# Optimization experiments

Hardware: AMD Instinct MI355X
Metric: run time of the kernel (lower is better)

## Reference

```python
import jax, jax.numpy as jnp
import numpy as np

N_QUBITS = 12
LAYERS = 3


def _apply(state, mats, axes):
    """Apply batched k-qubit gate. state: [B]+[2]*n complex64; mats: [B, 2^k, 2^k]; axes: state axes (1-based)."""
    k = len(axes)
    d = 2 ** k
    s = jnp.moveaxis(state, axes, tuple(range(1, k + 1)))
    shp = s.shape
    s = jnp.einsum('bij,bjk->bik', mats, s.reshape(shp[0], d, -1))
    return jnp.moveaxis(s.reshape(shp), tuple(range(1, k + 1)), axes)


def _ry(theta):
    # RY(theta) = [[cos(t/2), -sin(t/2)], [sin(t/2), cos(t/2)]], batched over B
    c = jnp.cos(theta / 2).astype(jnp.complex64)
    s = jnp.sin(theta / 2).astype(jnp.complex64)
    return jnp.stack([jnp.stack([c, -s], -1), jnp.stack([s, c], -1)], -2)


def _crx(theta):
    # CRX: identity on control=0 subspace, RX(theta) on control=1 subspace (basis order |ct>)
    c = jnp.cos(theta / 2).astype(jnp.complex64)
    s = (-1j) * jnp.sin(theta / 2).astype(jnp.complex64)
    o = jnp.ones_like(c)
    z = jnp.zeros_like(c)
    rows = [[o, z, z, z], [z, o, z, z], [z, z, c, s], [z, z, s, c]]
    return jnp.stack([jnp.stack(r, -1) for r in rows], -2)


def _circuit(state_re, state_im, params):
    B = params.shape[0]
    n = N_QUBITS
    state = (state_re + 1j * state_im).astype(jnp.complex64).reshape((B,) + (2,) * n)
    p = params.reshape(B, LAYERS, 4, n)  # param idx order: RY block, CRX block, RY block, CRX block
    for l in range(LAYERS):
        th = p[:, l]
        for w in range(n):
            state = _apply(state, _ry(th[:, 0, w]), (w + 1,))
        for i, w in enumerate(reversed(range(n))):
            state = _apply(state, _crx(th[:, 1, i]), (w + 1, ((w + 1) % n) + 1))
        for w in range(n):
            state = _apply(state, _ry(th[:, 2, w]), (w + 1,))
        for i, w in enumerate([n - 1] + list(range(n - 1))):
            state = _apply(state, _crx(th[:, 3, i]), (w + 1, ((w - 1) % n) + 1))
    state = state.reshape(B, -1)
    return jnp.stack([state.real, state.imag], -1)  # [B, 2^n, 2]


def setup_inputs() -> dict:
    key = jax.random.key(0)
    k1, k2, k3 = jax.random.split(key, 3)
    B = 128
    dim = 2 ** N_QUBITS
    return {
        'state_re': jax.random.normal(k1, (B, dim), jnp.float32),
        'state_im': jax.random.normal(k2, (B, dim), jnp.float32),
        'params': jax.random.normal(k3, (B, LAYERS * 4 * N_QUBITS), jnp.float32),
    }


def reference(state_re, state_im, params):
    return _circuit(state_re, state_im, params)
```

## Files before the change

### kernel.cpp

```cpp
#include <hip/hip_runtime.h>
#include <math.h>

#define DIM  4096
#define BLK  256
#define NPAR 144

typedef float v2f __attribute__((ext_vector_type(2)));

struct Ph { int reg[4]; int wav[2]; };
struct TMap { unsigned pk[8]; unsigned short so[16]; unsigned short rn[16]; };

constexpr int REGS[12][4] = {
  {8,9,10,11},
  {4,5,6,7},
  {0,1,2,3},
  {0,1,2,11},
  {2,3,4,5},
  {5,6,7,8},
  {8,9,10,11},
  {4,5,6,7},
  {0,1,10,11},
  {7,8,9,10},
  {4,5,6,7},
  {1,2,3,4}
};

constexpr Ph mkPh(int idx) {
  int l = idx / 12, e = idx % 12;
  Ph p = {};
  for (int j = 0; j < 4; ++j) p.reg[j] = REGS[e][j];
  int w0, w1;
  if (e == 11 || (l > 0 && e == 0)) { w0 = 0; w1 = 5; }
  else if (l == 0 && e <= 1)        { w0 = 0; w1 = 1; }
  else if (e <= 5)                  { w0 = 9; w1 = 10; }
  else                              { w0 = 2; w1 = 3; }
  p.wav[0] = w0; p.wav[1] = w1;
  return p;
}
constexpr Ph phaseAt(int i) {
  if (i == 0 || i == 37) { Ph p = {{0,1,2,3},{10,11}}; return p; }
  return mkPh(i - 1);
}
constexpr bool inArr(const int* a, int n, int b) {
  for (int i = 0; i < n; ++i) if (a[i] == b) return true;
  return false;
}
constexpr bool isLoc(int t) {
  if (t == 0 || t == 36) return false;
  Ph a = phaseAt(t), b = phaseAt(t + 1);
  return a.wav[0] == b.wav[0] && a.wav[1] == b.wav[1];
}
constexpr int bufIdx(int t) {
  int k = 0;
  for (int u = 0; u <= t; ++u) if (!isLoc(u)) ++k;
  return (k + 1) & 1;
}

struct BuildOut { TMap m; bool ok; };

constexpr BuildOut buildT(Ph o, Ph n, bool local) {
  BuildOut R = {};
  R.ok = true;
  bool lo[12] = {}, ln[12] = {};
  for (int b = 0; b < 12; ++b) {
    lo[b] = !inArr(o.reg, 4, b) && !inArr(o.wav, 2, b);
    ln[b] = !inArr(n.reg, 4, b) && !inArr(n.wav, 2, b);
  }
  int col[12] = {};
  bool uo[12] = {}, un[12] = {}, inBank[12] = {}, pairA[12] = {};
  int row = 0;
  for (int b = 0; b < 12 && row < 4; ++b)
    if (lo[b] && ln[b]) { col[b] |= 1 << row; uo[b] = un[b] = true; inBank[b] = true; ++row; }
  while (row < 4) {
    int a = -1, c = -1;
    for (int b = 0; b < 12; ++b) if (lo[b] && !uo[b]) { a = b; break; }
    for (int b = 0; b < 12; ++b) if (ln[b] && !un[b]) { c = b; break; }
    if (a < 0 || c < 0) { R.ok = false; return R; }
    col[a] |= 1 << row; col[c] |= 1 << row;
    uo[a] = true; un[c] = true; inBank[a] = true; inBank[c] = true; pairA[a] = true;
    ++row;
  }
  bool idset[12] = {};
  int nid = 0;
  for (int b = 0; b < 12; ++b) { idset[b] = !inBank[b] || pairA[b]; if (idset[b]) ++nid; }
  if (nid != 8) { R.ok = false; return R; }
  if (local) {
    if (!idset[o.wav[0]] || !idset[o.wav[1]]) { R.ok = false; return R; }
    col[o.wav[0]] |= 1 << 10; col[o.wav[1]] |= 1 << 11;
    idset[o.wav[0]] = idset[o.wav[1]] = false;
    int rr = 4;
    for (int b = 0; b < 12; ++b) if (idset[b]) { col[b] |= 1 << rr; ++rr; }
    if (rr != 10) { R.ok = false; return R; }
  } else {
    int rr = 4;
    for (int b = 0; b < 12; ++b) if (idset[b]) { col[b] |= 1 << rr; ++rr; }
    if (rr != 12) { R.ok = false; return R; }
  }
  {
    int pv[12] = {}, pb[12] = {};
    int nr = 0;
    for (int b = 0; b < 12; ++b) {
      int v = col[b];
      for (int k = 0; k < nr; ++k) if (v & pb[k]) v ^= pv[k];
      if (v) { pb[nr] = v & (-v); pv[nr] = v; ++nr; }
    }
    if (nr != 12) { R.ok = false; return R; }
  }
  int Lo[6] = {}, Ln[6] = {};
  int i0 = 0, i1 = 0;
  for (int b = 0; b < 12; ++b) { if (lo[b]) Lo[i0++] = b; if (ln[b]) Ln[i1++] = b; }
  for (int i = 0; i < 8; ++i) {
    unsigned po = (i < 6) ? (unsigned)col[Lo[i]] : (unsigned)col[o.wav[i - 6]];
    unsigned pn = (i < 6) ? (unsigned)col[Ln[i]] : (unsigned)col[n.wav[i - 6]];
    R.m.pk[i] = po | (pn << 16);
  }
  for (int r = 0; r < 16; ++r) {
    int s = 0, t = 0;
    for (int j = 0; j < 4; ++j)
      if ((r >> j) & 1) { s ^= col[o.reg[j]]; t ^= col[n.reg[j]]; }
    R.m.so[r] = (unsigned short)(s * 8);
    R.m.rn[r] = (unsigned short)(t * 8);
  }
  return R;
}

struct AllT { TMap t[37]; bool loc[37]; int buf[37]; bool ok; };
constexpr AllT buildAll() {
  AllT A = {};
  A.ok = true;
  for (int t = 0; t < 37; ++t) {
    BuildOut b = buildT(phaseAt(t), phaseAt(t + 1), isLoc(t));
    A.t[t] = b.m;
    A.ok = A.ok && b.ok;
    A.loc[t] = isLoc(t);
    A.buf[t] = bufIdx(t);
  }
  return A;
}
constexpr AllT AT = buildAll();
static_assert(AT.ok, "slot-map construction failed");

template<int J>
__device__ __forceinline__ void ry16(v2f (&z)[16], v2f a) {
  const float c = a.x, s = a.y;
  #pragma unroll
  for (int p = 0; p < 8; ++p) {
    const int r0 = ((p & ~((1 << J) - 1)) << 1) | (p & ((1 << J) - 1));
    const int r1 = r0 | (1 << J);
    v2f u = z[r0], v = z[r1];
    z[r0] = c * u - s * v;
    z[r1] = s * u + c * v;
  }
}
template<int JC, int JT>
__device__ __forceinline__ void crx16(v2f (&z)[16], v2f a) {
  const float c = a.x, s = a.y;
  constexpr int MC = 1 << JC, MT = 1 << JT;
  constexpr int mlo = MC < MT ? MC : MT;
  constexpr int mhi = MC < MT ? MT : MC;
  #pragma unroll
  for (int p = 0; p < 4; ++p) {
    int q = ((p & ~(mlo - 1)) << 1) | (p & (mlo - 1));
    q = ((q & ~(mhi - 1)) << 1) | (q & (mhi - 1));
    const int r0 = q | MC, r1 = r0 | MT;
    v2f u = z[r0], v = z[r1];
    v2f n0, n1;
    n0.x = c * u.x + s * v.y;
    n0.y = c * u.y - s * v.x;
    n1.x = c * v.x + s * u.y;
    n1.y = c * v.y - s * u.x;
    z[r0] = n0; z[r1] = n1;
  }
}

template<int E>
__device__ __forceinline__ void gates(v2f (&z)[16], const v2f* ang, int base) {
  auto A = [&](int k) { return ang[base + k]; };
  if constexpr (E == 0)      { ry16<0>(z,A(3));  ry16<1>(z,A(2));  ry16<2>(z,A(1));  ry16<3>(z,A(0)); }
  else if constexpr (E == 1) { ry16<0>(z,A(7));  ry16<1>(z,A(6));  ry16<2>(z,A(5));  ry16<3>(z,A(4)); }
  else if constexpr (E == 2) { ry16<0>(z,A(11)); ry16<1>(z,A(10)); ry16<2>(z,A(9));  ry16<3>(z,A(8)); }
  else if constexpr (E == 3) { crx16<0,3>(z,A(12)); crx16<1,0>(z,A(13)); crx16<2,1>(z,A(14)); }
  else if constexpr (E == 4) { crx16<1,0>(z,A(15)); crx16<2,1>(z,A(16)); crx16<3,2>(z,A(17)); }
  else if constexpr (E == 5) { crx16<1,0>(z,A(18)); crx16<2,1>(z,A(19)); crx16<3,2>(z,A(20)); }
  else if constexpr (E == 6) { crx16<1,0>(z,A(21)); crx16<2,1>(z,A(22)); crx16<3,2>(z,A(23));
                               ry16<0>(z,A(27)); ry16<1>(z,A(26)); }
  else if constexpr (E == 7) { ry16<0>(z,A(31)); ry16<1>(z,A(30)); ry16<2>(z,A(29)); ry16<3>(z,A(28)); }
  else if constexpr (E == 8) { ry16<2>(z,A(25)); ry16<3>(z,A(24)); ry16<0>(z,A(35)); ry16<1>(z,A(34));
                               crx16<0,1>(z,A(36)); crx16<3,0>(z,A(37)); crx16<2,3>(z,A(38)); }
  else if constexpr (E == 9) { crx16<2,3>(z,A(39)); crx16<1,2>(z,A(40)); crx16<0,1>(z,A(41)); }
  else if constexpr (E == 10){ crx16<2,3>(z,A(42)); crx16<1,2>(z,A(43)); crx16<0,1>(z,A(44)); }
  else                       { ry16<1>(z,A(33)); ry16<2>(z,A(32));
                               crx16<2,3>(z,A(45)); crx16<1,2>(z,A(46)); crx16<0,1>(z,A(47)); }
}

template<int T>
__device__ __forceinline__ void restage(v2f (&z)[16], int tid, char* Lb, char* C0, char* C1) {
  constexpr bool LOC = AT.loc[T];
  char* buf = LOC ? Lb : (AT.buf[T] ? C1 : C0);
  unsigned acc = 0;
  #pragma unroll
  for (int i = 0; i < 8; ++i)
    acc ^= (unsigned)(-((tid >> i) & 1)) & AT.t[T].pk[i];
  const unsigned bo = (acc & 0xfffu) << 3;
  const unsigned bn = ((acc >> 16) & 0xfffu) << 3;
  #pragma unroll
  for (int r = 0; r < 16; ++r)
    *(v2f*)(buf + (bo ^ AT.t[T].so[r])) = z[r];
  if (LOC) { asm volatile("s_waitcnt lgkmcnt(0)" ::: "memory"); }
  else     { __syncthreads(); }
  #pragma unroll
  for (int r = 0; r < 16; ++r)
    z[r] = *(const v2f*)(buf + (bn ^ AT.t[T].rn[r]));
}

template<int L>
__device__ __forceinline__ void layer(v2f (&z)[16], int tid, const v2f* ang,
                                      char* Lb, char* C0, char* C1) {
  const int base = 48 * L;
  gates<0>(z, ang, base);  restage<12*L + 1>(z, tid, Lb, C0, C1);
  gates<1>(z, ang, base);  restage<12*L + 2>(z, tid, Lb, C0, C1);
  gates<2>(z, ang, base);  restage<12*L + 3>(z, tid, Lb, C0, C1);
  gates<3>(z, ang, base);  restage<12*L + 4>(z, tid, Lb, C0, C1);
  gates<4>(z, ang, base);  restage<12*L + 5>(z, tid, Lb, C0, C1);
  gates<5>(z, ang, base);  restage<12*L + 6>(z, tid, Lb, C0, C1);
  gates<6>(z, ang, base);  restage<12*L + 7>(z, tid, Lb, C0, C1);
  gates<7>(z, ang, base);  restage<12*L + 8>(z, tid, Lb, C0, C1);
  gates<8>(z, ang, base);  restage<12*L + 9>(z, tid, Lb, C0, C1);
  gates<9>(z, ang, base);  restage<12*L + 10>(z, tid, Lb, C0, C1);
  gates<10>(z, ang, base); restage<12*L + 11>(z, tid, Lb, C0, C1);
  gates<11>(z, ang, base);
  if constexpr (L < 2) restage<12*L + 12>(z, tid, Lb, C0, C1);
}

__global__ __launch_bounds__(BLK) void ansatz_kernel(
    const float* __restrict__ sre, const float* __restrict__ sim,
    const float* __restrict__ params, float* __restrict__ out) {

  __shared__ v2f C0s[DIM], C1s[DIM], Ls[DIM];
  __shared__ v2f ang[NPAR];

  const int b = blockIdx.x, tid = threadIdx.x;
  char* C0 = (char*)C0s;
  char* C1 = (char*)C1s;
  char* Lb = (char*)Ls;

  if (tid < NPAR) {
    float s, c;
    sincosf(0.5f * params[b * NPAR + tid], &s, &c);
    v2f a; a.x = c; a.y = s;
    ang[tid] = a;
  }

  v2f z[16];
  {
    const float4* pr = (const float4*)(sre + b * DIM + (tid << 4));
    const float4* pi = (const float4*)(sim + b * DIM + (tid << 4));
    float4 fr[4], fi[4];
    #pragma unroll
    for (int k = 0; k < 4; ++k) { fr[k] = pr[k]; fi[k] = pi[k]; }
    unsigned acc = 0;
    #pragma unroll
    for (int i = 0; i < 8; ++i)
      acc ^= (unsigned)(-((tid >> i) & 1)) & AT.t[0].pk[i];
    const unsigned bo = (acc & 0xfffu) << 3;
    const unsigned bn = ((acc >> 16) & 0xfffu) << 3;
    #pragma unroll
    for (int r = 0; r < 16; ++r) {
      const float* f0 = (const float*)&fr[r >> 2];
      const float* f1 = (const float*)&fi[r >> 2];
      v2f v; v.x = f0[r & 3]; v.y = f1[r & 3];
      *(v2f*)(C0 + (bo ^ AT.t[0].so[r])) = v;
    }
    __syncthreads();
    #pragma unroll
    for (int r = 0; r < 16; ++r)
      z[r] = *(const v2f*)(C0 + (bn ^ AT.t[0].rn[r]));
  }

  layer<0>(z, tid, ang, Lb, C0, C1);
  layer<1>(z, tid, ang, Lb, C0, C1);
  layer<2>(z, tid, ang, Lb, C0, C1);

  {
    unsigned acc = 0;
    #pragma unroll
    for (int i = 0; i < 8; ++i)
      acc ^= (unsigned)(-((tid >> i) & 1)) & AT.t[36].pk[i];
    const unsigned bo = (acc & 0xfffu) << 3;
    const unsigned bn = ((acc >> 16) & 0xfffu) << 3;
    char* buf = AT.buf[36] ? C1 : C0;
    #pragma unroll
    for (int r = 0; r < 16; ++r)
      *(v2f*)(buf + (bo ^ AT.t[36].so[r])) = z[r];
    __syncthreads();
    v2f* o2 = (v2f*)out + (size_t)b * DIM + (tid << 4);
    #pragma unroll
    for (int r = 0; r < 16; r += 2) {
      v2f v0 = *(const v2f*)(buf + (bn ^ AT.t[36].rn[r]));
      v2f v1 = *(const v2f*)(buf + (bn ^ AT.t[36].rn[r + 1]));
      float4 w; w.x = v0.x; w.y = v0.y; w.z = v1.x; w.w = v1.y;
      *(float4*)(o2 + r) = w;
    }
  }
}

extern "C" void kernel_launch(void* const* d_in, const int* in_sizes, int n_in,
                              void* d_out, int out_size, void* d_ws, size_t ws_size,
                              hipStream_t stream) {
  const float* sre    = (const float*)d_in[0];
  const float* sim    = (const float*)d_in[1];
  const float* params = (const float*)d_in[2];
  float* out          = (float*)d_out;

  const int B = in_sizes[0] / DIM;
  ansatz_kernel<<<B, BLK, 0, stream>>>(sre, sim, params, out);
}
```

Baseline: 90.67 us.

## Split state across 512 threads with 3-qubit register phases

Doubles the block size to 512 threads so each thread holds 8 amplitudes (3 register qubits) instead of 16, with three wave-level qubits instead of two. The phase schedule is redesigned around sliding 3-qubit windows, so each phase applies a few RY/CRX gates before restaging through shared memory, and the compile-time slot-map builder is generalised to match. This exposes more parallelism per block and cuts register pressure. In exchange there are the same number of restage phases, each doing less arithmetic, so LDS traffic and barrier cost per gate rise relative to compute.

```diff
diff --git a/kernel.cpp b/kernel.cpp
--- a/kernel.cpp
+++ b/kernel.cpp
@@ -2,44 +2,30 @@
 #include <math.h>
 
 #define DIM  4096
-#define BLK  256
+#define BLK  512
 #define NPAR 144
 
 typedef float v2f __attribute__((ext_vector_type(2)));
 
-struct Ph { int reg[4]; int wav[2]; };
-struct TMap { unsigned pk[8]; unsigned short so[16]; unsigned short rn[16]; };
-
-constexpr int REGS[12][4] = {
-  {8,9,10,11},
-  {4,5,6,7},
-  {0,1,2,3},
-  {0,1,2,11},
-  {2,3,4,5},
-  {5,6,7,8},
-  {8,9,10,11},
-  {4,5,6,7},
-  {0,1,10,11},
-  {7,8,9,10},
-  {4,5,6,7},
-  {1,2,3,4}
-};
-
-constexpr Ph mkPh(int idx) {
-  int l = idx / 12, e = idx % 12;
+struct Ph { int reg[3]; int wav[3]; };
+struct TMap { unsigned pk[9]; unsigned short so[8]; unsigned short rn[8]; };
+
+constexpr int REGS[12][3] = {
+  {11,0,1},{1,2,3},{3,4,5},{5,6,7},{7,8,9},{9,10,11},
+  {11,0,1},{9,10,11},{7,8,9},{5,6,7},{3,4,5},{1,2,3}};
+
+constexpr Ph phaseAt(int i) {
   Ph p = {};
-  for (int j = 0; j < 4; ++j) p.reg[j] = REGS[e][j];
-  int w0, w1;
-  if (e == 11 || (l > 0 && e == 0)) { w0 = 0; w1 = 5; }
-  else if (l == 0 && e <= 1)        { w0 = 0; w1 = 1; }
-  else if (e <= 5)                  { w0 = 9; w1 = 10; }
-  else                              { w0 = 2; w1 = 3; }
-  p.wav[0] = w0; p.wav[1] = w1;
+  if (i == 0 || i == 37) {
+    p.reg[0]=0; p.reg[1]=1; p.reg[2]=2;
+    p.wav[0]=9; p.wav[1]=10; p.wav[2]=11;
+    return p;
+  }
+  int e = (i - 1) % 12;
+  for (int j = 0; j < 3; ++j) p.reg[j] = REGS[e][j];
+  bool A = (e <= 2) || (e >= 10);
+  p.wav[0] = A ? 6 : 2; p.wav[1] = A ? 7 : 3; p.wav[2] = A ? 8 : 4;
   return p;
-}
-constexpr Ph phaseAt(int i) {
-  if (i == 0 || i == 37) { Ph p = {{0,1,2,3},{10,11}}; return p; }
-  return mkPh(i - 1);
 }
 constexpr bool inArr(const int* a, int n, int b) {
   for (int i = 0; i < n; ++i) if (a[i] == b) return true;
@@ -48,7 +34,7 @@
 constexpr bool isLoc(int t) {
   if (t == 0 || t == 36) return false;
   Ph a = phaseAt(t), b = phaseAt(t + 1);
-  return a.wav[0] == b.wav[0] && a.wav[1] == b.wav[1];
+  return a.wav[0]==b.wav[0] && a.wav[1]==b.wav[1] && a.wav[2]==b.wav[2];
 }
 constexpr int bufIdx(int t) {
   int k = 0;
@@ -63,21 +49,21 @@
   R.ok = true;
   bool lo[12] = {}, ln[12] = {};
   for (int b = 0; b < 12; ++b) {
-    lo[b] = !inArr(o.reg, 4, b) && !inArr(o.wav, 2, b);
-    ln[b] = !inArr(n.reg, 4, b) && !inArr(n.wav, 2, b);
+    lo[b] = !inArr(o.reg,3,b) && !inArr(o.wav,3,b);
+    ln[b] = !inArr(n.reg,3,b) && !inArr(n.wav,3,b);
   }
   int col[12] = {};
   bool uo[12] = {}, un[12] = {}, inBank[12] = {}, pairA[12] = {};
   int row = 0;
   for (int b = 0; b < 12 && row < 4; ++b)
-    if (lo[b] && ln[b]) { col[b] |= 1 << row; uo[b] = un[b] = true; inBank[b] = true; ++row; }
+    if (lo[b] && ln[b]) { col[b] |= 1 << row; uo[b]=un[b]=true; inBank[b]=true; ++row; }
   while (row < 4) {
     int a = -1, c = -1;
     for (int b = 0; b < 12; ++b) if (lo[b] && !uo[b]) { a = b; break; }
     for (int b = 0; b < 12; ++b) if (ln[b] && !un[b]) { c = b; break; }
-    if (a < 0 || c < 0) { R.ok = false; return R; }
+    if (a < 0 || c < 0 || a == c) { R.ok = false; return R; }
     col[a] |= 1 << row; col[c] |= 1 << row;
-    uo[a] = true; un[c] = true; inBank[a] = true; inBank[c] = true; pairA[a] = true;
+    uo[a]=true; un[c]=true; inBank[a]=true; inBank[c]=true; pairA[a]=true;
     ++row;
   }
   bool idset[12] = {};
@@ -85,12 +71,14 @@
   for (int b = 0; b < 12; ++b) { idset[b] = !inBank[b] || pairA[b]; if (idset[b]) ++nid; }
   if (nid != 8) { R.ok = false; return R; }
   if (local) {
-    if (!idset[o.wav[0]] || !idset[o.wav[1]]) { R.ok = false; return R; }
-    col[o.wav[0]] |= 1 << 10; col[o.wav[1]] |= 1 << 11;
-    idset[o.wav[0]] = idset[o.wav[1]] = false;
+    for (int i = 0; i < 3; ++i) {
+      if (!idset[o.wav[i]]) { R.ok = false; return R; }
+      col[o.wav[i]] |= 1 << (9 + i);
+      idset[o.wav[i]] = false;
+    }
     int rr = 4;
     for (int b = 0; b < 12; ++b) if (idset[b]) { col[b] |= 1 << rr; ++rr; }
-    if (rr != 10) { R.ok = false; return R; }
+    if (rr != 9) { R.ok = false; return R; }
   } else {
     int rr = 4;
     for (int b = 0; b < 12; ++b) if (idset[b]) { col[b] |= 1 << rr; ++rr; }
@@ -109,17 +97,17 @@
   int Lo[6] = {}, Ln[6] = {};
   int i0 = 0, i1 = 0;
   for (int b = 0; b < 12; ++b) { if (lo[b]) Lo[i0++] = b; if (ln[b]) Ln[i1++] = b; }
-  for (int i = 0; i < 8; ++i) {
-    unsigned po = (i < 6) ? (unsigned)col[Lo[i]] : (unsigned)col[o.wav[i - 6]];
-    unsigned pn = (i < 6) ? (unsigned)col[Ln[i]] : (unsigned)col[n.wav[i - 6]];
+  for (int i = 0; i < 9; ++i) {
+    unsigned po = (i < 6) ? (unsigned)col[Lo[i]] : (unsigned)col[o.wav[i-6]];
+    unsigned pn = (i < 6) ? (unsigned)col[Ln[i]] : (unsigned)col[n.wav[i-6]];
     R.m.pk[i] = po | (pn << 16);
   }
-  for (int r = 0; r < 16; ++r) {
-    int s = 0, t = 0;
-    for (int j = 0; j < 4; ++j)
-      if ((r >> j) & 1) { s ^= col[o.reg[j]]; t ^= col[n.reg[j]]; }
+  for (int r = 0; r < 8; ++r) {
+    int s = 0, t2 = 0;
+    for (int j = 0; j < 3; ++j)
+      if ((r >> j) & 1) { s ^= col[o.reg[j]]; t2 ^= col[n.reg[j]]; }
     R.m.so[r] = (unsigned short)(s * 8);
-    R.m.rn[r] = (unsigned short)(t * 8);
+    R.m.rn[r] = (unsigned short)(t2 * 8);
   }
   return R;
 }
@@ -141,10 +129,10 @@
 static_assert(AT.ok, "slot-map construction failed");
 
 template<int J>
-__device__ __forceinline__ void ry16(v2f (&z)[16], v2f a) {
+__device__ __forceinline__ void ry8(v2f (&z)[8], v2f a) {
   const float c = a.x, s = a.y;
   #pragma unroll
-  for (int p = 0; p < 8; ++p) {
+  for (int p = 0; p < 4; ++p) {
     const int r0 = ((p & ~((1 << J) - 1)) << 1) | (p & ((1 << J) - 1));
     const int r1 = r0 | (1 << J);
     v2f u = z[r0], v = z[r1];
@@ -153,13 +141,13 @@
   }
 }
 template<int JC, int JT>
-__device__ __forceinline__ void crx16(v2f (&z)[16], v2f a) {
+__device__ __forceinline__ void crx8(v2f (&z)[8], v2f a) {
   const float c = a.x, s = a.y;
   constexpr int MC = 1 << JC, MT = 1 << JT;
   constexpr int mlo = MC < MT ? MC : MT;
   constexpr int mhi = MC < MT ? MT : MC;
   #pragma unroll
-  for (int p = 0; p < 4; ++p) {
+  for (int p = 0; p < 2; ++p) {
     int q = ((p & ~(mlo - 1)) << 1) | (p & (mlo - 1));
     q = ((q & ~(mhi - 1)) << 1) | (q & (mhi - 1));
     const int r0 = q | MC, r1 = r0 | MT;
@@ -174,47 +162,56 @@
 }
 
 template<int E>
-__device__ __forceinline__ void gates(v2f (&z)[16], const v2f* ang, int base) {
+__device__ __forceinline__ void gates(v2f (&z)[8], const v2f* ang, int base) {
   auto A = [&](int k) { return ang[base + k]; };
-  if constexpr (E == 0)      { ry16<0>(z,A(3));  ry16<1>(z,A(2));  ry16<2>(z,A(1));  ry16<3>(z,A(0)); }
-  else if constexpr (E == 1) { ry16<0>(z,A(7));  ry16<1>(z,A(6));  ry16<2>(z,A(5));  ry16<3>(z,A(4)); }
-  else if constexpr (E == 2) { ry16<0>(z,A(11)); ry16<1>(z,A(10)); ry16<2>(z,A(9));  ry16<3>(z,A(8)); }
-  else if constexpr (E == 3) { crx16<0,3>(z,A(12)); crx16<1,0>(z,A(13)); crx16<2,1>(z,A(14)); }
-  else if constexpr (E == 4) { crx16<1,0>(z,A(15)); crx16<2,1>(z,A(16)); crx16<3,2>(z,A(17)); }
-  else if constexpr (E == 5) { crx16<1,0>(z,A(18)); crx16<2,1>(z,A(19)); crx16<3,2>(z,A(20)); }
-  else if constexpr (E == 6) { crx16<1,0>(z,A(21)); crx16<2,1>(z,A(22)); crx16<3,2>(z,A(23));
-                               ry16<0>(z,A(27)); ry16<1>(z,A(26)); }
-  else if constexpr (E == 7) { ry16<0>(z,A(31)); ry16<1>(z,A(30)); ry16<2>(z,A(29)); ry16<3>(z,A(28)); }
-  else if constexpr (E == 8) { ry16<2>(z,A(25)); ry16<3>(z,A(24)); ry16<0>(z,A(35)); ry16<1>(z,A(34));
-                               crx16<0,1>(z,A(36)); crx16<3,0>(z,A(37)); crx16<2,3>(z,A(38)); }
-  else if constexpr (E == 9) { crx16<2,3>(z,A(39)); crx16<1,2>(z,A(40)); crx16<0,1>(z,A(41)); }
-  else if constexpr (E == 10){ crx16<2,3>(z,A(42)); crx16<1,2>(z,A(43)); crx16<0,1>(z,A(44)); }
-  else                       { ry16<1>(z,A(33)); ry16<2>(z,A(32));
-                               crx16<2,3>(z,A(45)); crx16<1,2>(z,A(46)); crx16<0,1>(z,A(47)); }
+  if constexpr (E == 0)      { ry8<0>(z,A(0));  ry8<1>(z,A(11)); ry8<2>(z,A(10));
+                               crx8<1,0>(z,A(12)); crx8<2,1>(z,A(13)); }
+  else if constexpr (E == 1) { ry8<1>(z,A(9));  ry8<2>(z,A(8));
+                               crx8<1,0>(z,A(14)); crx8<2,1>(z,A(15)); }
+  else if constexpr (E == 2) { ry8<1>(z,A(7));  ry8<2>(z,A(6));
+                               crx8<1,0>(z,A(16)); crx8<2,1>(z,A(17)); }
+  else if constexpr (E == 3) { ry8<1>(z,A(5));  ry8<2>(z,A(4));
+                               crx8<1,0>(z,A(18)); crx8<2,1>(z,A(19)); }
+  else if constexpr (E == 4) { ry8<1>(z,A(3));  ry8<2>(z,A(2));
+                               crx8<1,0>(z,A(20)); crx8<2,1>(z,A(21)); }
+  else if constexpr (E == 5) { ry8<1>(z,A(1));
+                               crx8<1,0>(z,A(22)); crx8<2,1>(z,A(23)); }
+  else if constexpr (E == 6) { ry8<0>(z,A(24)); ry8<1>(z,A(35)); ry8<2>(z,A(34));
+                               crx8<1,2>(z,A(36)); crx8<0,1>(z,A(37)); }
+  else if constexpr (E == 7) { ry8<0>(z,A(26)); ry8<1>(z,A(25));
+                               crx8<1,2>(z,A(38)); crx8<0,1>(z,A(39)); }
+  else if constexpr (E == 8) { ry8<0>(z,A(28)); ry8<1>(z,A(27));
+                               crx8<1,2>(z,A(40)); crx8<0,1>(z,A(41)); }
+  else if constexpr (E == 9) { ry8<0>(z,A(30)); ry8<1>(z,A(29));
+                               crx8<1,2>(z,A(42)); crx8<0,1>(z,A(43)); }
+  else if constexpr (E == 10){ ry8<0>(z,A(32)); ry8<1>(z,A(31));
+                               crx8<1,2>(z,A(44)); crx8<0,1>(z,A(45)); }
+  else                       { ry8<1>(z,A(33));
+                               crx8<1,2>(z,A(46)); crx8<0,1>(z,A(47)); }
 }
 
 template<int T>
-__device__ __forceinline__ void restage(v2f (&z)[16], int tid, char* Lb, char* C0, char* C1) {
+__device__ __forceinline__ void restage(v2f (&z)[8], int tid, char* Lb, char* C0, char* C1) {
   constexpr bool LOC = AT.loc[T];
   char* buf = LOC ? Lb : (AT.buf[T] ? C1 : C0);
   unsigned acc = 0;
   #pragma unroll
-  for (int i = 0; i < 8; ++i)
+  for (int i = 0; i < 9; ++i)
     acc ^= (unsigned)(-((tid >> i) & 1)) & AT.t[T].pk[i];
   const unsigned bo = (acc & 0xfffu) << 3;
   const unsigned bn = ((acc >> 16) & 0xfffu) << 3;
   #pragma unroll
-  for (int r = 0; r < 16; ++r)
+  for (int r = 0; r < 8; ++r)
     *(v2f*)(buf + (bo ^ AT.t[T].so[r])) = z[r];
   if (LOC) { asm volatile("s_waitcnt lgkmcnt(0)" ::: "memory"); }
   else     { __syncthreads(); }
   #pragma unroll
-  for (int r = 0; r < 16; ++r)
+  for (int r = 0; r < 8; ++r)
     z[r] = *(const v2f*)(buf + (bn ^ AT.t[T].rn[r]));
 }
 
 template<int L>
-__device__ __forceinline__ void layer(v2f (&z)[16], int tid, const v2f* ang,
+__device__ __forceinline__ void layer(v2f (&z)[8], int tid, const v2f* ang,
                                       char* Lb, char* C0, char* C1) {
   const int base = 48 * L;
   gates<0>(z, ang, base);  restage<12*L + 1>(z, tid, Lb, C0, C1);
@@ -251,21 +248,21 @@
     ang[tid] = a;
   }
 
-  v2f z[16];
+  v2f z[8];
   {
-    const float4* pr = (const float4*)(sre + b * DIM + (tid << 4));
-    const float4* pi = (const float4*)(sim + b * DIM + (tid << 4));
-    float4 fr[4], fi[4];
-    #pragma unroll
-    for (int k = 0; k < 4; ++k) { fr[k] = pr[k]; fi[k] = pi[k]; }
+    const float4* pr = (const float4*)(sre + b * DIM + (tid << 3));
+    const float4* pi = (const float4*)(sim + b * DIM + (tid << 3));
+    float4 fr[2], fi[2];
+    fr[0] = pr[0]; fr[1] = pr[1];
+    fi[0] = pi[0]; fi[1] = pi[1];
     unsigned acc = 0;
     #pragma unroll
-    for (int i = 0; i < 8; ++i)
+    for (int i = 0; i < 9; ++i)
       acc ^= (unsigned)(-((tid >> i) & 1)) & AT.t[0].pk[i];
     const unsigned bo = (acc & 0xfffu) << 3;
     const unsigned bn = ((acc >> 16) & 0xfffu) << 3;
     #pragma unroll
-    for (int r = 0; r < 16; ++r) {
+    for (int r = 0; r < 8; ++r) {
       const float* f0 = (const float*)&fr[r >> 2];
       const float* f1 = (const float*)&fi[r >> 2];
       v2f v; v.x = f0[r & 3]; v.y = f1[r & 3];
@@ -273,7 +270,7 @@
     }
     __syncthreads();
     #pragma unroll
-    for (int r = 0; r < 16; ++r)
+    for (int r = 0; r < 8; ++r)
       z[r] = *(const v2f*)(C0 + (bn ^ AT.t[0].rn[r]));
   }
 
@@ -284,18 +281,18 @@
   {
     unsigned acc = 0;
     #pragma unroll
-    for (int i = 0; i < 8; ++i)
+    for (int i = 0; i < 9; ++i)
       acc ^= (unsigned)(-((tid >> i) & 1)) & AT.t[36].pk[i];
     const unsigned bo = (acc & 0xfffu) << 3;
     const unsigned bn = ((acc >> 16) & 0xfffu) << 3;
     char* buf = AT.buf[36] ? C1 : C0;
     #pragma unroll
-    for (int r = 0; r < 16; ++r)
+    for (int r = 0; r < 8; ++r)
       *(v2f*)(buf + (bo ^ AT.t[36].so[r])) = z[r];
     __syncthreads();
-    v2f* o2 = (v2f*)out + (size_t)b * DIM + (tid << 4);
-    #pragma unroll
-    for (int r = 0; r < 16; r += 2) {
+    v2f* o2 = (v2f*)out + (size_t)b * DIM + (tid << 3);
+    #pragma unroll
+    for (int r = 0; r < 8; r += 2) {
       v2f v0 = *(const v2f*)(buf + (bn ^ AT.t[36].rn[r]));
       v2f v1 = *(const v2f*)(buf + (bn ^ AT.t[36].rn[r + 1]));
       float4 w; w.x = v0.x; w.y = v0.y; w.z = v1.x; w.w = v1.y;
```

Result: faster. 84.11 us (-7.2%).
